# Performance work log

Measured on AMD Instinct MI355X. Metric: run time of the kernel, lower is better.

Reference implementation:

```python
import jax, jax.numpy as jnp
import numpy as np

D_MODEL = 1024
N_HEADS = 16
HEAD_DIM = D_MODEL // N_HEADS  # 64
BATCH, SEQ = 2, 2048
MASK_FILL = -1000000000.0


def setup_inputs() -> dict:
    key = jax.random.key(0)
    ks = jax.random.split(key, 13)
    s = 1.0 / np.sqrt(D_MODEL)
    inp = {
        "q": jax.random.normal(ks[0], (BATCH, SEQ, D_MODEL), jnp.float32),
        "k": jax.random.normal(ks[1], (BATCH, SEQ, D_MODEL), jnp.float32),
        "v": jax.random.normal(ks[2], (BATCH, SEQ, D_MODEL), jnp.float32),
        "mask": jax.random.randint(ks[3], (BATCH, 1, SEQ, SEQ), 0, 2, jnp.int32),
        "Wq": jax.random.normal(ks[4], (D_MODEL, D_MODEL), jnp.float32) * s,
        "bq": jax.random.normal(ks[5], (D_MODEL,), jnp.float32) * s,
        "Wk": jax.random.normal(ks[6], (D_MODEL, D_MODEL), jnp.float32) * s,
        "bk": jax.random.normal(ks[7], (D_MODEL,), jnp.float32) * s,
        "Wv": jax.random.normal(ks[8], (D_MODEL, D_MODEL), jnp.float32) * s,
        "bv": jax.random.normal(ks[9], (D_MODEL,), jnp.float32) * s,
        "Wo": jax.random.normal(ks[10], (D_MODEL, D_MODEL), jnp.float32) * s,
        "bo": jax.random.normal(ks[11], (D_MODEL,), jnp.float32) * s,
    }
    return inp


def reference(q, k, v, mask, Wq, bq, Wk, bk, Wv, bv, Wo, bo):
    batch, seq, feat = q.shape
    # Linear projections (torch Linear: x @ W.T + b)
    qp = q @ Wq.T + bq
    kp = k @ Wk.T + bk
    vp = v @ Wv.T + bv

    def split(x):
        # (B, S, D) -> (B, H, S, Dh)
        return x.reshape(batch, seq, N_HEADS, HEAD_DIM).swapaxes(1, 2)

    qh, kh, vh = split(qp), split(kp), split(vp)

    # (B, H, S, S) score matrix, scaled
    score = jnp.einsum("bhqd,bhkd->bhqk", qh, kh) / jnp.sqrt(
        jnp.asarray(HEAD_DIM, qh.dtype))
    score = jnp.where(mask == 0, jnp.asarray(MASK_FILL, score.dtype), score)
    attn = jax.nn.softmax(score, axis=-1)
    out = jnp.einsum("bhqk,bhkd->bhqd", attn, vh)  # (B, H, S, Dh)
    joint = out.swapaxes(1, 2).reshape(batch, seq, feat)
    return joint @ Wo.T + bo
```

## Files before the change

### kernel.cpp

```cpp
#include <hip/hip_runtime.h>

typedef unsigned short u16;
typedef unsigned int u32;
typedef unsigned long long u64;
typedef float f32x4 __attribute__((ext_vector_type(4)));
typedef float f32x16 __attribute__((ext_vector_type(16)));
typedef __bf16 bf16x4 __attribute__((ext_vector_type(4)));
typedef __bf16 bf16x8 __attribute__((ext_vector_type(8)));
typedef u16 u16x8 __attribute__((ext_vector_type(8)));
typedef u32 u32x4 __attribute__((ext_vector_type(4)));

#define QSCALE 0.18033688011112042f

__device__ __forceinline__ u16 f2bf(float f) {
  unsigned int u = __float_as_uint(f);
  u += 0x7fffu + ((u >> 16) & 1u);
  return (u16)(u >> 16);
}

__device__ __forceinline__ void async16(const void* g, void* l) {
  __builtin_amdgcn_global_load_lds(
      (__attribute__((address_space(1))) void*)g,
      (__attribute__((address_space(3))) void*)l,
      16, 0, 0);
}

__device__ __forceinline__ f32x4 mfma16(bf16x8 a, bf16x8 b, f32x4 c) {
  return __builtin_amdgcn_mfma_f32_16x16x32_bf16(a, b, c, 0, 0, 0);
}

__device__ __forceinline__ f32x16 mfma32(bf16x8 a, bf16x8 b, f32x16 c) {
  return __builtin_amdgcn_mfma_f32_32x32x16_bf16(a, b, c, 0, 0, 0);
}

__device__ __forceinline__ u32 cvtpk(float lo, float hi) {
  u32 r;
  asm("v_cvt_pk_bf16_f32 %0, %1, %2" : "=v"(r) : "v"(lo), "v"(hi));
  return r;
}

__device__ __forceinline__ void pswap(u32& a, u32& b) {
  asm("v_permlane32_swap_b32 %0, %1" : "+v"(a), "+v"(b));
}

struct CvtArgs {
  const float* src[7];
  u16* dst[7];
};

__global__ __launch_bounds__(256) void cvt_kernel(CvtArgs a) {
  int z = blockIdx.z;
  int n = (z < 3) ? 4194304 : 1048576;
  int base = (blockIdx.x * 256 + threadIdx.x) * 8;
  if (base >= n) return;
  const float* s = a.src[z] + base;
  f32x4 x0 = *(const f32x4*)s;
  f32x4 x1 = *(const f32x4*)(s + 4);
  u16x8 pk;
  pk[0]=f2bf(x0[0]); pk[1]=f2bf(x0[1]); pk[2]=f2bf(x0[2]); pk[3]=f2bf(x0[3]);
  pk[4]=f2bf(x1[0]); pk[5]=f2bf(x1[1]); pk[6]=f2bf(x1[2]); pk[7]=f2bf(x1[3]);
  *(u16x8*)(a.dst[z] + base) = pk;
}

__global__ __launch_bounds__(256) void pack_mask_kernel(
    const int* __restrict__ mask, u64* __restrict__ pm) {
  int idx = blockIdx.x * 256 + threadIdx.x;
  const int4* src = (const int4*)(mask + (size_t)idx * 64);
  u64 bits = 0ull;
#pragma unroll
  for (int j = 0; j < 16; ++j) {
    int4 v = src[j];
    if (v.x) bits |= 1ull << (4 * j + 0);
    if (v.y) bits |= 1ull << (4 * j + 1);
    if (v.z) bits |= 1ull << (4 * j + 2);
    if (v.w) bits |= 1ull << (4 * j + 3);
  }
  pm[idx] = bits;
}

__device__ __forceinline__ void gemm_body(const u16* __restrict__ A,
                                          const u16* __restrict__ W,
                                          const float* __restrict__ bias,
                                          void* __restrict__ outraw, int mode,
                                          float oscale) {
  alignas(16) __shared__ u16 lA[128 * 32];
  alignas(16) __shared__ u16 lB[128 * 32];
  const int tid = threadIdx.x;
  const int lane = tid & 63, wv = tid >> 6;
  const int wm = wv >> 1, wn = wv & 1;
  const int m0 = blockIdx.y * 128, n0 = blockIdx.x * 128;
  const int l15 = lane & 15, quad = lane >> 4;
  const int srow = lane >> 2;
  const int scol = (lane & 3) * 8;

  f32x4 acc[4][4] = {};

  for (int k0 = 0; k0 < 1024; k0 += 32) {
#pragma unroll
    for (int t = 0; t < 2; ++t) {
      int rb = (wv * 2 + t) * 16;
      async16(A + (size_t)(m0 + rb + srow) * 1024 + k0 + scol, (char*)lA + rb * 64);
      async16(W + (size_t)(n0 + rb + srow) * 1024 + k0 + scol, (char*)lB + rb * 64);
    }
    __syncthreads();
    bf16x8 af[4], bfr[4];
#pragma unroll
    for (int i = 0; i < 4; ++i) {
      af[i]  = *(const bf16x8*)(lA + (wm * 64 + i * 16 + l15) * 32 + quad * 8);
      bfr[i] = *(const bf16x8*)(lB + (wn * 64 + i * 16 + l15) * 32 + quad * 8);
    }
#pragma unroll
    for (int i = 0; i < 4; ++i)
#pragma unroll
      for (int j = 0; j < 4; ++j)
        acc[i][j] = mfma16(af[i], bfr[j], acc[i][j]);
    __syncthreads();
  }

#pragma unroll
  for (int i = 0; i < 4; ++i) {
    int mbase = m0 + wm * 64 + i * 16 + quad * 4;
#pragma unroll
    for (int j = 0; j < 4; ++j) {
      int n = n0 + wn * 64 + j * 16 + l15;
      float bv = bias[n];
#pragma unroll
      for (int r = 0; r < 4; ++r) {
        int m = mbase + r;
        float val = (acc[i][j][r] + bv) * oscale;
        if (mode == 0) {
          int b = m >> 11, s = m & 2047, h = n >> 6, dh = n & 63;
          ((u16*)outraw)[((((size_t)b * 16 + h) * 2048 + s) << 6) + dh] = f2bf(val);
        } else if (mode == 1) {
          int b = m >> 11, s = m & 2047, h = n >> 6, dh = n & 63;
          ((u16*)outraw)[((((size_t)b * 16 + h) * 64 + dh) << 11) + s] = f2bf(val);
        } else {
          ((float*)outraw)[(size_t)m * 1024 + n] = val;
        }
      }
    }
  }
}

__global__ __launch_bounds__(256) void gemm_qkv_kernel(
    const u16* __restrict__ qb, const u16* __restrict__ kb, const u16* __restrict__ vb,
    const u16* __restrict__ Wqb, const float* __restrict__ bq,
    const u16* __restrict__ Wkb, const float* __restrict__ bk,
    const u16* __restrict__ Wvb, const float* __restrict__ bv,
    u16* __restrict__ qp, u16* __restrict__ kp, u16* __restrict__ vt) {
  if (blockIdx.z == 0)      gemm_body(qb, Wqb, bq, qp, 0, QSCALE);
  else if (blockIdx.z == 1) gemm_body(kb, Wkb, bk, kp, 0, 1.0f);
  else                      gemm_body(vb, Wvb, bv, vt, 1, 1.0f);
}

__global__ __launch_bounds__(256) void gemm_o_kernel(
    const u16* __restrict__ joint, const u16* __restrict__ Wob,
    const float* __restrict__ bo, float* __restrict__ out) {
  gemm_body(joint, Wob, bo, out, 2, 1.0f);
}

__global__ __launch_bounds__(256, 4) void attn_kernel(
    const u16* __restrict__ qp, const u16* __restrict__ kp,
    const u16* __restrict__ vt, const u64* __restrict__ pm,
    u16* __restrict__ joint) {
  alignas(16) __shared__ char smem[32768];

  const int tid = threadIdx.x, lane = tid & 63, wv = tid >> 6;
  const int l31 = lane & 31, hi = lane >> 5, l7 = lane & 7;
  const int qg = wv >> 1, kh = wv & 1;

  const int linear = blockIdx.x;
  const int xcd = linear & 7, slot = linear >> 3;
  const int grp = (xcd << 2) | (slot >> 5);
  const int q0 = (slot & 31) * 64;
  const int hd = grp & 15, b = grp >> 4;

  const size_t head_off = ((size_t)b * 16 + hd) * 2048 * 64;
  const u16* Qh = qp + head_off;
  const u16* Kh = kp + head_off;
  const u16* Vh = vt + head_off;
  const int qr = q0 + qg * 32 + l31;
  const u32* pmq32 = (const u32*)(pm + ((size_t)b * 2048 + qr) * 32) + kh;

  bf16x8 qf[4];
  {
    const u16* qrow = Qh + (size_t)qr * 64 + hi * 8;
#pragma unroll
    for (int d = 0; d < 4; ++d) qf[d] = *(const bf16x8*)(qrow + d * 16);
  }

  const int sd0 = tid, sd1 = 256 + tid;
  const int kr0 = sd0 >> 3, ks0 = ((sd0 & 7) ^ (kr0 & 7)) * 8;
  const int kr1 = sd1 >> 3, ks1 = ((sd1 & 7) ^ (kr1 & 7)) * 8;
  const u16* kg0 = Kh + (size_t)kr0 * 64 + ks0;
  const u16* kg1 = Kh + (size_t)kr1 * 64 + ks1;
  const u16* vg0 = Vh + (size_t)kr0 * 2048 + ks0;
  const u16* vg1 = Vh + (size_t)kr1 * 2048 + ks1;

  f32x16 O[2] = {};
  f32x4 lacc = {};
  const f32x16 fz16 = {};

  async16(kg0, smem + sd0 * 16);
  async16(kg1, smem + sd1 * 16);
  async16(vg0, smem + 16384 + sd0 * 16);
  async16(vg1, smem + 16384 + sd1 * 16);

  for (int kt = 0; kt < 32; ++kt) {
    __syncthreads();

    if (kt != 31) {
      const size_t kadv = (size_t)(kt + 1) * 4096;
      const int vadv = (kt + 1) * 64;
      char* kd = smem + (((kt + 1) & 1) << 13);
      char* vd = smem + 16384 + (((kt + 1) & 1) << 13);
      async16(kg0 + kadv, kd + sd0 * 16);
      async16(kg1 + kadv, kd + sd1 * 16);
      async16(vg0 + vadv, vd + sd0 * 16);
      async16(vg1 + vadv, vd + sd1 * 16);
    }

    u32 wh = pmq32[2 * kt];
    const char* kc = smem + ((kt & 1) << 13);
    const char* vc = smem + 16384 + ((kt & 1) << 13);

    bf16x8 kf[4];
#pragma unroll
    for (int d = 0; d < 4; ++d)
      kf[d] = *(const bf16x8*)(kc + (kh * 32 + l31) * 128 +
                               (((2 * d + hi) ^ l7) << 4));

    f32x16 S;
    {
      f32x16 s = mfma32(kf[0], qf[0], fz16);
      s = mfma32(kf[1], qf[1], s);
      s = mfma32(kf[2], qf[2], s);
      S = mfma32(kf[3], qf[3], s);
    }

    bf16x8 vf[2][2];
#pragma unroll
    for (int g = 0; g < 2; ++g)
#pragma unroll
      for (int t = 0; t < 2; ++t) {
        int ks = kh * 2 + t;
        vf[g][t] = *(const bf16x8*)(vc + (g * 32 + l31) * 128 +
                                    (((2 * ks + hi) ^ l7) << 4));
      }

    {
      const int hi4 = hi * 4;
#pragma unroll
      for (int rq = 0; rq < 4; ++rq) {
        u32 nib = wh >> (rq * 8 + hi4);
#pragma unroll
        for (int r4 = 0; r4 < 4; ++r4) {
          int i = rq * 4 + r4;
          float pe = __builtin_amdgcn_exp2f(S[i]);
          S[i] = ((nib >> r4) & 1u) ? pe : 0.f;
        }
        f32x4 sv = {S[rq * 4 + 0], S[rq * 4 + 1], S[rq * 4 + 2], S[rq * 4 + 3]};
        lacc += sv;
      }
    }

    bf16x8 pf[2];
#pragma unroll
    for (int t = 0; t < 2; ++t) {
      int ra = t * 8;
      u32 w0a = cvtpk(S[ra + 0], S[ra + 1]);
      u32 w1a = cvtpk(S[ra + 2], S[ra + 3]);
      u32 w0b = cvtpk(S[ra + 4], S[ra + 5]);
      u32 w1b = cvtpk(S[ra + 6], S[ra + 7]);
      pswap(w0a, w0b);
      pswap(w1a, w1b);
      u32x4 tt = {w0a, w1a, w0b, w1b};
      pf[t] = __builtin_bit_cast(bf16x8, tt);
    }

#pragma unroll
    for (int g = 0; g < 2; ++g) {
      f32x16 o = O[g];
      o = mfma32(vf[g][0], pf[0], o);
      O[g] = mfma32(vf[g][1], pf[1], o);
    }
  }

  float lp = (lacc[0] + lacc[1]) + (lacc[2] + lacc[3]);
  lp += __shfl_xor(lp, 32, 64);
  __syncthreads();
  float* exch = (float*)smem;
  if (kh == 1) {
    float* e = exch + (qg * 64 + lane) * 34;
#pragma unroll
    for (int g = 0; g < 2; ++g)
#pragma unroll
      for (int i = 0; i < 16; ++i) e[g * 16 + i] = O[g][i];
    e[32] = lp;
  }
  __syncthreads();
  if (kh == 0) {
    const float* e = exch + (qg * 64 + lane) * 34;
#pragma unroll
    for (int g = 0; g < 2; ++g)
#pragma unroll
      for (int i = 0; i < 16; ++i) O[g][i] += e[g * 16 + i];
    lp += e[32];
    float inv = 1.0f / lp;
    size_t row_off = ((size_t)b * 2048 + qr) * 1024 + hd * 64;
#pragma unroll
    for (int g = 0; g < 2; ++g)
#pragma unroll
      for (int rq = 0; rq < 4; ++rq) {
        f32x4 ov = {O[g][rq * 4 + 0] * inv, O[g][rq * 4 + 1] * inv,
                    O[g][rq * 4 + 2] * inv, O[g][rq * 4 + 3] * inv};
        bf16x4 obv = __builtin_convertvector(ov, bf16x4);
        *(u64*)(joint + row_off + g * 32 + rq * 8 + hi * 4) =
            *(const u64*)&obv;
      }
  }
}

extern "C" void kernel_launch(void* const* d_in, const int* in_sizes, int n_in,
                              void* d_out, int out_size, void* d_ws, size_t ws_size,
                              hipStream_t stream) {
  const float* q  = (const float*)d_in[0];
  const float* k  = (const float*)d_in[1];
  const float* v  = (const float*)d_in[2];
  const int* mask = (const int*)d_in[3];
  const float* Wq = (const float*)d_in[4];
  const float* bq = (const float*)d_in[5];
  const float* Wk = (const float*)d_in[6];
  const float* bk = (const float*)d_in[7];
  const float* Wv = (const float*)d_in[8];
  const float* bv = (const float*)d_in[9];
  const float* Wo = (const float*)d_in[10];
  const float* bo = (const float*)d_in[11];
  float* out = (float*)d_out;

  u16* w = (u16*)d_ws;
  u16* qp    = w;
  u16* kp    = w + 4194304;
  u16* vt    = w + 8388608;
  u16* qb    = w + 12582912;
  u16* kb    = w + 16777216;
  u16* vb    = w + 20971520;
  u16* Wqb   = w + 25165824;
  u16* Wkb   = w + 26214400;
  u16* Wvb   = w + 27262976;
  u16* Wob   = w + 28311552;
  u64* pm    = (u64*)(w + 29360128);
  u16* joint = qb;

  CvtArgs ca;
  ca.src[0] = q;  ca.dst[0] = qb;
  ca.src[1] = k;  ca.dst[1] = kb;
  ca.src[2] = v;  ca.dst[2] = vb;
  ca.src[3] = Wq; ca.dst[3] = Wqb;
  ca.src[4] = Wk; ca.dst[4] = Wkb;
  ca.src[5] = Wv; ca.dst[5] = Wvb;
  ca.src[6] = Wo; ca.dst[6] = Wob;

  pack_mask_kernel<<<dim3(512), dim3(256), 0, stream>>>(mask, pm);
  cvt_kernel<<<dim3(2048, 1, 7), dim3(256), 0, stream>>>(ca);
  gemm_qkv_kernel<<<dim3(8, 32, 3), dim3(256), 0, stream>>>(
      qb, kb, vb, Wqb, bq, Wkb, bk, Wvb, bv, qp, kp, vt);
  attn_kernel<<<dim3(1024), dim3(256), 0, stream>>>(qp, kp, vt, pm, joint);
  gemm_o_kernel<<<dim3(8, 32, 1), dim3(256), 0, stream>>>(joint, Wob, bo, out);
}
```

Measured before the change: 272.2 us.

## Double attention block to 128 queries so eight waves share K/V tiles

The attention block grows to 512 threads covering 128 query rows, so each K/V tile staged into LDS serves four query groups instead of two. Each thread now issues one async load per tile instead of two, and the block-to-head mapping is rewritten for the 512-block grid. MFMA sections are wrapped in s_setprio to favour matrix issue. The final cross-wave reduction is split into two halves so the exchange buffer fits in the 32 KB LDS. The larger block trades occupancy flexibility and adds extra barriers in the epilogue.

```diff
diff --git a/kernel.cpp b/kernel.cpp
--- a/kernel.cpp
+++ b/kernel.cpp
@@ -159,7 +159,7 @@
   gemm_body(joint, Wob, bo, out, 2, 1.0f);
 }
 
-__global__ __launch_bounds__(256, 4) void attn_kernel(
+__global__ __launch_bounds__(512, 2) void attn_kernel(
     const u16* __restrict__ qp, const u16* __restrict__ kp,
     const u16* __restrict__ vt, const u64* __restrict__ pm,
     u16* __restrict__ joint) {
@@ -169,10 +169,9 @@
   const int l31 = lane & 31, hi = lane >> 5, l7 = lane & 7;
   const int qg = wv >> 1, kh = wv & 1;
 
-  const int linear = blockIdx.x;
-  const int xcd = linear & 7, slot = linear >> 3;
-  const int grp = (xcd << 2) | (slot >> 5);
-  const int q0 = (slot & 31) * 64;
+  const int bid = blockIdx.x;
+  const int grp = ((bid & 7) << 2) | ((bid >> 3) & 3);
+  const int q0 = (bid >> 5) * 128;
   const int hd = grp & 15, b = grp >> 4;
 
   const size_t head_off = ((size_t)b * 16 + hd) * 2048 * 64;
@@ -189,22 +188,17 @@
     for (int d = 0; d < 4; ++d) qf[d] = *(const bf16x8*)(qrow + d * 16);
   }
 
-  const int sd0 = tid, sd1 = 256 + tid;
-  const int kr0 = sd0 >> 3, ks0 = ((sd0 & 7) ^ (kr0 & 7)) * 8;
-  const int kr1 = sd1 >> 3, ks1 = ((sd1 & 7) ^ (kr1 & 7)) * 8;
-  const u16* kg0 = Kh + (size_t)kr0 * 64 + ks0;
-  const u16* kg1 = Kh + (size_t)kr1 * 64 + ks1;
-  const u16* vg0 = Vh + (size_t)kr0 * 2048 + ks0;
-  const u16* vg1 = Vh + (size_t)kr1 * 2048 + ks1;
+  const int sd = tid;
+  const int kr = sd >> 3, ks = ((sd & 7) ^ (kr & 7)) * 8;
+  const u16* kg = Kh + (size_t)kr * 64 + ks;
+  const u16* vg = Vh + (size_t)kr * 2048 + ks;
 
   f32x16 O[2] = {};
   f32x4 lacc = {};
   const f32x16 fz16 = {};
 
-  async16(kg0, smem + sd0 * 16);
-  async16(kg1, smem + sd1 * 16);
-  async16(vg0, smem + 16384 + sd0 * 16);
-  async16(vg1, smem + 16384 + sd1 * 16);
+  async16(kg, smem + sd * 16);
+  async16(vg, smem + 16384 + sd * 16);
 
   for (int kt = 0; kt < 32; ++kt) {
     __syncthreads();
@@ -214,10 +208,8 @@
       const int vadv = (kt + 1) * 64;
       char* kd = smem + (((kt + 1) & 1) << 13);
       char* vd = smem + 16384 + (((kt + 1) & 1) << 13);
-      async16(kg0 + kadv, kd + sd0 * 16);
-      async16(kg1 + kadv, kd + sd1 * 16);
-      async16(vg0 + vadv, vd + sd0 * 16);
-      async16(vg1 + vadv, vd + sd1 * 16);
+      async16(kg + kadv, kd + sd * 16);
+      async16(vg + vadv, vd + sd * 16);
     }
 
     u32 wh = pmq32[2 * kt];
@@ -232,10 +224,12 @@
 
     f32x16 S;
     {
+      __builtin_amdgcn_s_setprio(1);
       f32x16 s = mfma32(kf[0], qf[0], fz16);
       s = mfma32(kf[1], qf[1], s);
       s = mfma32(kf[2], qf[2], s);
       S = mfma32(kf[3], qf[3], s);
+      __builtin_amdgcn_s_setprio(0);
     }
 
     bf16x8 vf[2][2];
@@ -243,9 +237,9 @@
     for (int g = 0; g < 2; ++g)
 #pragma unroll
       for (int t = 0; t < 2; ++t) {
-        int ks = kh * 2 + t;
+        int vks = kh * 2 + t;
         vf[g][t] = *(const bf16x8*)(vc + (g * 32 + l31) * 128 +
-                                    (((2 * ks + hi) ^ l7) << 4));
+                                    (((2 * vks + hi) ^ l7) << 4));
       }
 
     {
@@ -278,34 +272,41 @@
       pf[t] = __builtin_bit_cast(bf16x8, tt);
     }
 
+    __builtin_amdgcn_s_setprio(1);
 #pragma unroll
     for (int g = 0; g < 2; ++g) {
       f32x16 o = O[g];
       o = mfma32(vf[g][0], pf[0], o);
       O[g] = mfma32(vf[g][1], pf[1], o);
     }
+    __builtin_amdgcn_s_setprio(0);
   }
 
   float lp = (lacc[0] + lacc[1]) + (lacc[2] + lacc[3]);
   lp += __shfl_xor(lp, 32, 64);
   __syncthreads();
   float* exch = (float*)smem;
+  float* e = exch + (qg * 64 + lane) * 17;
   if (kh == 1) {
-    float* e = exch + (qg * 64 + lane) * 34;
-#pragma unroll
-    for (int g = 0; g < 2; ++g)
-#pragma unroll
-      for (int i = 0; i < 16; ++i) e[g * 16 + i] = O[g][i];
-    e[32] = lp;
+#pragma unroll
+    for (int i = 0; i < 16; ++i) e[i] = O[0][i];
+    e[16] = lp;
   }
   __syncthreads();
   if (kh == 0) {
-    const float* e = exch + (qg * 64 + lane) * 34;
-#pragma unroll
-    for (int g = 0; g < 2; ++g)
-#pragma unroll
-      for (int i = 0; i < 16; ++i) O[g][i] += e[g * 16 + i];
-    lp += e[32];
+#pragma unroll
+    for (int i = 0; i < 16; ++i) O[0][i] += e[i];
+    lp += e[16];
+  }
+  __syncthreads();
+  if (kh == 1) {
+#pragma unroll
+    for (int i = 0; i < 16; ++i) e[i] = O[1][i];
+  }
+  __syncthreads();
+  if (kh == 0) {
+#pragma unroll
+    for (int i = 0; i < 16; ++i) O[1][i] += e[i];
     float inv = 1.0f / lp;
     size_t row_off = ((size_t)b * 2048 + qr) * 1024 + hd * 64;
 #pragma unroll
@@ -365,6 +366,6 @@
   cvt_kernel<<<dim3(2048, 1, 7), dim3(256), 0, stream>>>(ca);
   gemm_qkv_kernel<<<dim3(8, 32, 3), dim3(256), 0, stream>>>(
       qb, kb, vb, Wqb, bq, Wkb, bk, Wvb, bv, qp, kp, vt);
-  attn_kernel<<<dim3(1024), dim3(256), 0, stream>>>(qp, kp, vt, pm, joint);
+  attn_kernel<<<dim3(512), dim3(512), 0, stream>>>(qp, kp, vt, pm, joint);
   gemm_o_kernel<<<dim3(8, 32, 1), dim3(256), 0, stream>>>(joint, Wob, bo, out);
 }
```

After: 273.6 us. No clear change (+0.5%).
